# Performance work log

Measured on AMD Instinct MI355X. Metric: run time of the kernel, lower is better.

## Reference

```python
import jax, jax.numpy as jnp
import numpy as np
import math

D_MODEL = 1024
N_HEADS = 16
D_K = D_MODEL // N_HEADS
LN_EPS = 1e-5


def _linear_params(key, d_in, d_out):
    # torch Linear stores weight as [out, in]; xavier_uniform init
    bound = math.sqrt(6.0 / (d_in + d_out))
    kw, kb = jax.random.split(key)
    W = jax.random.uniform(kw, (d_out, d_in), jnp.float32, -bound, bound)
    b = jnp.zeros((d_out,), jnp.float32)
    return W, b


def setup_inputs() -> dict:
    key = jax.random.key(0)
    ks = jax.random.split(key, 8)
    x = jax.random.normal(ks[0], (2, 2048, D_MODEL), jnp.float32)
    reasoning_state = jax.random.normal(ks[1], (2, D_MODEL), jnp.float32)
    Wq, bq = _linear_params(ks[2], D_MODEL, D_MODEL)
    Wk, bk = _linear_params(ks[3], D_MODEL, D_MODEL)
    Wv, bv = _linear_params(ks[4], D_MODEL, D_MODEL)
    Wr, br = _linear_params(ks[5], D_MODEL, D_MODEL)
    Wo, bo = _linear_params(ks[6], D_MODEL, D_MODEL)
    ln_g = jnp.ones((D_MODEL,), jnp.float32)
    ln_b = jnp.zeros((D_MODEL,), jnp.float32)
    return {"x": x, "reasoning_state": reasoning_state,
            "Wq": Wq, "bq": bq, "Wk": Wk, "bk": bk, "Wv": Wv, "bv": bv,
            "Wr": Wr, "br": br, "Wo": Wo, "bo": bo, "ln_g": ln_g, "ln_b": ln_b}


def reference(x, reasoning_state, Wq, bq, Wk, bk, Wv, bv, Wr, br, Wo, bo, ln_g, ln_b):
    B, S, D = x.shape
    H, dk = N_HEADS, D_K

    def proj(z, W, b):  # torch Linear: z @ W.T + b
        return z @ W.T + b

    # [B, H, S, dk]
    Q = proj(x, Wq, bq).reshape(B, S, H, dk).transpose(0, 2, 1, 3)
    K = proj(x, Wk, bk).reshape(B, S, H, dk).transpose(0, 2, 1, 3)
    V = proj(x, Wv, bv).reshape(B, S, H, dk).transpose(0, 2, 1, 3)

    scores = jnp.einsum('bhsd,bhtd->bhst', Q, K) / math.sqrt(dk)

    # reasoning bias: R is [B, H, 1, dk]; Q @ R^T -> [B, H, S, 1], broadcast over keys
    R = proj(reasoning_state, Wr, br).reshape(B, 1, H, dk).transpose(0, 2, 1, 3)
    scores = scores + jnp.einsum('bhsd,bhud->bhsu', Q, R)  # u == 1, broadcasts

    attn = jax.nn.softmax(scores, axis=-1)
    context = jnp.einsum('bhst,bhtd->bshd', attn, V).reshape(B, S, D)
    out = proj(context, Wo, bo)

    # residual + LayerNorm
    y = out + x
    mu = jnp.mean(y, axis=-1, keepdims=True)
    var = jnp.var(y, axis=-1, keepdims=True)
    y = (y - mu) * jax.lax.rsqrt(var + LN_EPS) * ln_g + ln_b
    return (y, attn)
```

## Files before the change

### kernel.cpp

```cpp
#include <hip/hip_runtime.h>
#include <hip/hip_bf16.h>

#define DM 1024
#define NH 16
#define DKK 64
#define SL 2048
#define NBATCH 2
#define NR (NBATCH*SL)

typedef __attribute__((ext_vector_type(8))) __bf16 bf16x8;
typedef __attribute__((ext_vector_type(4))) float f32x4;
using bf16 = __hip_bfloat16;

#define QSCALE 0.18033688011112042f

#define LGKM_BARRIER() do { \
  asm volatile("s_waitcnt lgkmcnt(0)" ::: "memory"); \
  __builtin_amdgcn_s_barrier(); \
  __builtin_amdgcn_sched_barrier(0); \
} while (0)

__global__ __launch_bounds__(256) void cvt_kernel(const float* __restrict__ src,
                                                  bf16* __restrict__ dst, int n4) {
  int stride = gridDim.x * blockDim.x;
  for (int i = blockIdx.x * blockDim.x + threadIdx.x; i < n4; i += stride) {
    float4 v = ((const float4*)src)[i];
    union { bf16 h[4]; ushort4 u; } un;
    un.h[0] = __float2bfloat16(v.x);
    un.h[1] = __float2bfloat16(v.y);
    un.h[2] = __float2bfloat16(v.z);
    un.h[3] = __float2bfloat16(v.w);
    ((ushort4*)dst)[i] = un.u;
  }
}

__global__ __launch_bounds__(256) void cvt4_kernel(
    const float* __restrict__ s0, const float* __restrict__ s1,
    const float* __restrict__ s2, const float* __restrict__ s3,
    bf16* __restrict__ d0, bf16* __restrict__ d1,
    bf16* __restrict__ d2, bf16* __restrict__ d3) {
  const int z = blockIdx.y;
  const float* src = (z == 0) ? s0 : (z == 1) ? s1 : (z == 2) ? s2 : s3;
  bf16* dst = (z == 0) ? d0 : (z == 1) ? d1 : (z == 2) ? d2 : d3;
  const int n4 = DM * DM / 4;
  int stride = gridDim.x * blockDim.x;
  for (int i = blockIdx.x * blockDim.x + threadIdx.x; i < n4; i += stride) {
    float4 v = ((const float4*)src)[i];
    union { bf16 h[4]; ushort4 u; } un;
    un.h[0] = __float2bfloat16(v.x);
    un.h[1] = __float2bfloat16(v.y);
    un.h[2] = __float2bfloat16(v.z);
    un.h[3] = __float2bfloat16(v.w);
    ((ushort4*)dst)[i] = un.u;
  }
}

__device__ __forceinline__ void gemm_core(const bf16* __restrict__ A, const bf16* __restrict__ W,
                                          int rowStart, int colStart,
                                          bf16* As, bf16* Bs, f32x4 acc[4][4]) {
  const int t = threadIdx.x;
  const int lane = t & 63, w = t >> 6;
  const int lg = lane & 15, lh = lane >> 4;
  const int wm = (w >> 1) * 64, wn = (w & 1) * 64;
#pragma unroll
  for (int i = 0; i < 4; ++i)
#pragma unroll
    for (int j = 0; j < 4; ++j) acc[i][j] = (f32x4){0.f, 0.f, 0.f, 0.f};

  for (int kt = 0; kt < DM / 32; ++kt) {
    int kb = kt * 32;
#pragma unroll
    for (int q = 0; q < 2; ++q) {
      int idx = q * 256 + t;
      int row = idx >> 2;
      int ce = (idx & 3) * 8;
      const bf16* ga = A + (size_t)(rowStart + row) * DM + kb + ce;
      const bf16* gb = W + (size_t)(colStart + row) * DM + kb + ce;
      int ldsbase = (q * 256 + w * 64) * 8;
      __builtin_amdgcn_global_load_lds((const __attribute__((address_space(1))) void*)ga,
                                       (__attribute__((address_space(3))) void*)(As + ldsbase),
                                       16, 0, 0);
      __builtin_amdgcn_global_load_lds((const __attribute__((address_space(1))) void*)gb,
                                       (__attribute__((address_space(3))) void*)(Bs + ldsbase),
                                       16, 0, 0);
    }
    __syncthreads();
    bf16x8 af[4], bfr[4];
#pragma unroll
    for (int i = 0; i < 4; ++i)
      af[i] = *(const bf16x8*)(As + (wm + i * 16 + lg) * 32 + 8 * lh);
#pragma unroll
    for (int j = 0; j < 4; ++j)
      bfr[j] = *(const bf16x8*)(Bs + (wn + j * 16 + lg) * 32 + 8 * lh);
#pragma unroll
    for (int i = 0; i < 4; ++i)
#pragma unroll
      for (int j = 0; j < 4; ++j)
        acc[i][j] = __builtin_amdgcn_mfma_f32_16x16x32_bf16(af[i], bfr[j], acc[i][j], 0, 0, 0);
    __syncthreads();
  }
}

__global__ __launch_bounds__(256) void gemm_qkv_kernel(
    const bf16* __restrict__ xb,
    const bf16* __restrict__ Wqb, const bf16* __restrict__ Wkb, const bf16* __restrict__ Wvb,
    const float* __restrict__ bq, const float* __restrict__ bk, const float* __restrict__ bv,
    bf16* __restrict__ Qb, bf16* __restrict__ Kb, bf16* __restrict__ Vt) {
  __shared__ bf16 smem[128 * 128];
  bf16* As = smem;
  bf16* Bs = smem + 4096;
  const int z = blockIdx.z;
  const bf16* W = (z == 0) ? Wqb : (z == 1) ? Wkb : Wvb;
  const float* bias = (z == 0) ? bq : (z == 1) ? bk : bv;
  int rowStart = blockIdx.y * 128, colStart = blockIdx.x * 128;
  f32x4 acc[4][4];
  gemm_core(xb, W, rowStart, colStart, As, Bs, acc);

  const int t = threadIdx.x, lane = t & 63, w = t >> 6;
  const int lg = lane & 15, lh = lane >> 4;
  const int wm = (w >> 1) * 64, wn = (w & 1) * 64;
  if (z < 2) {
    bf16* out = (z == 0) ? Qb : Kb;
    const float sc = (z == 0) ? QSCALE : 1.0f;
#pragma unroll
    for (int i = 0; i < 4; ++i)
#pragma unroll
      for (int j = 0; j < 4; ++j) {
        int col = colStart + wn + j * 16 + lg;
        float bb = bias[col];
#pragma unroll
        for (int r = 0; r < 4; ++r) {
          int row = rowStart + wm + i * 16 + 4 * lh + r;
          out[(size_t)row * DM + col] = __float2bfloat16((acc[i][j][r] + bb) * sc);
        }
      }
  } else {
    char* T = (char*)smem;
    __syncthreads();
#pragma unroll
    for (int i = 0; i < 4; ++i)
#pragma unroll
      for (int j = 0; j < 4; ++j) {
        int col = wn + j * 16 + lg;
        float bb = bias[colStart + col];
        const int swz = (col & 7) << 4;
#pragma unroll
        for (int r2 = 0; r2 < 4; r2 += 2) {
          int row = wm + i * 16 + 4 * lh + r2;
          union { bf16 hh[2]; unsigned u; } un;
          un.hh[0] = __float2bfloat16(acc[i][j][r2] + bb);
          un.hh[1] = __float2bfloat16(acc[i][j][r2 + 1] + bb);
          *(unsigned*)(T + ((col * 256 + row * 2) ^ swz)) = un.u;
        }
      }
    __syncthreads();
    const int b_i = rowStart >> 11;
    const int sbase = rowStart & 2047;
#pragma unroll
    for (int rd = 0; rd < 8; ++rd) {
      int d_loc = rd * 16 + (t >> 4);
      int s8 = (t & 15) * 8;
      bf16x8 v = *(const bf16x8*)(T + ((d_loc * 256 + s8 * 2) ^ ((d_loc & 7) << 4)));
      int col = colStart + d_loc;
      int h2 = col >> 6, d = col & 63;
      *(bf16x8*)(Vt + ((size_t)(b_i * NH + h2) * DKK + d) * SL + sbase + s8) = v;
    }
  }
}

__global__ __launch_bounds__(256) void attn_den_kernel(
    const bf16* __restrict__ Qb, const bf16* __restrict__ Kb,
    float* __restrict__ linv_g) {
  __shared__ float sl[2 * 128];
  const int t = threadIdx.x, lane = t & 63, w = t >> 6;
  const int lg = lane & 15, lh = lane >> 4;
  const int L = blockIdx.x;
  const int xcd = L & 7, s_in = L >> 3;
  const int bh = xcd * 4 + (s_in >> 4);
  const int qtile = s_in & 15;
  const int b = bh >> 4, h = bh & 15;
  const int qbase = qtile * 128;
  const int wr = w >> 1, wc = w & 1;

  bf16x8 qf[4][2];
#pragma unroll
  for (int i = 0; i < 4; ++i)
#pragma unroll
    for (int ks = 0; ks < 2; ++ks)
      qf[i][ks] = *(const bf16x8*)(Qb +
          (size_t)(b * SL + qbase + wr * 64 + i * 16 + lg) * DM + h * DKK + ks * 32 + 8 * lh);

  const bf16* Kbase = Kb + (size_t)b * SL * DM + h * DKK;

  float lsum[4] = {0.f, 0.f, 0.f, 0.f};
  for (int kt = 0; kt < 16; ++kt) {
    bf16x8 kf[4][2];
#pragma unroll
    for (int j = 0; j < 4; ++j)
#pragma unroll
      for (int ks = 0; ks < 2; ++ks)
        kf[j][ks] = *(const bf16x8*)(Kbase +
            (size_t)(kt * 128 + wc * 64 + j * 16 + lg) * DM + ks * 32 + 8 * lh);
#pragma unroll
    for (int i = 0; i < 4; ++i) {
      f32x4 s[4];
      __builtin_amdgcn_s_setprio(1);
#pragma unroll
      for (int j = 0; j < 4; ++j) {
        f32x4 z = (f32x4){0.f, 0.f, 0.f, 0.f};
        z = __builtin_amdgcn_mfma_f32_16x16x32_bf16(kf[j][0], qf[i][0], z, 0, 0, 0);
        s[j] = __builtin_amdgcn_mfma_f32_16x16x32_bf16(kf[j][1], qf[i][1], z, 0, 0, 0);
      }
      __builtin_amdgcn_s_setprio(0);
#pragma unroll
      for (int j = 0; j < 4; ++j)
#pragma unroll
        for (int r = 0; r < 4; ++r) lsum[i] += exp2f(s[j][r]);
      __builtin_amdgcn_sched_barrier(0);
    }
  }
#pragma unroll
  for (int i = 0; i < 4; ++i) {
    lsum[i] += __shfl_xor(lsum[i], 16);
    lsum[i] += __shfl_xor(lsum[i], 32);
  }
  if (lh == 0) {
#pragma unroll
    for (int i = 0; i < 4; ++i) sl[wc * 128 + wr * 64 + i * 16 + lg] = lsum[i];
  }
  __syncthreads();
  if (t < 128) {
    linv_g[(size_t)bh * SL + qbase + t] = 1.f / (sl[t] + sl[128 + t]);
  }
}

__global__ __launch_bounds__(256) void attn_wr_kernel(
    const bf16* __restrict__ Qb, const bf16* __restrict__ Kb, const bf16* __restrict__ Vt,
    const float* __restrict__ linv_g,
    float* __restrict__ attn_out, bf16* __restrict__ ctxb) {
  __shared__ bf16 Ps[128 * 128];
  const int t = threadIdx.x, lane = t & 63, w = t >> 6;
  const int lg = lane & 15, lh = lane >> 4;
  const int L = blockIdx.x;
  const int xcd = L & 7, s_in = L >> 3;
  const int bh = xcd * 4 + (s_in >> 4);
  const int qtile = s_in & 15;
  const int b = bh >> 4, h = bh & 15;
  const int qbase = qtile * 128;
  const int wr = w >> 1, wc = w & 1;

  bf16x8 qf[4][2];
#pragma unroll
  for (int i = 0; i < 4; ++i)
#pragma unroll
    for (int ks = 0; ks < 2; ++ks)
      qf[i][ks] = *(const bf16x8*)(Qb +
          (size_t)(b * SL + qbase + wr * 64 + i * 16 + lg) * DM + h * DKK + ks * 32 + 8 * lh);

  float linv[4];
#pragma unroll
  for (int i = 0; i < 4; ++i)
    linv[i] = linv_g[(size_t)bh * SL + qbase + wr * 64 + i * 16 + lg];

  const bf16* Kbase = Kb + (size_t)b * SL * DM + h * DKK;
  const bf16* Vtb = Vt + (size_t)bh * DKK * SL;
  float* attn_base = attn_out + (size_t)bh * SL * SL;
  char* Pb = (char*)Ps;

  f32x4 cacc[4][2];
#pragma unroll
  for (int i = 0; i < 4; ++i) {
    cacc[i][0] = (f32x4){0.f, 0.f, 0.f, 0.f};
    cacc[i][1] = (f32x4){0.f, 0.f, 0.f, 0.f};
  }

  for (int kt = 0; kt < 16; ++kt) {
    bf16x8 kf[4][2];
#pragma unroll
    for (int j = 0; j < 4; ++j)
#pragma unroll
      for (int ks = 0; ks < 2; ++ks)
        kf[j][ks] = *(const bf16x8*)(Kbase +
            (size_t)(kt * 128 + wc * 64 + j * 16 + lg) * DM + ks * 32 + 8 * lh);

    LGKM_BARRIER();

#pragma unroll
    for (int i = 0; i < 4; ++i) {
      f32x4 s[4];
      __builtin_amdgcn_s_setprio(1);
#pragma unroll
      for (int j = 0; j < 4; ++j) {
        f32x4 z = (f32x4){0.f, 0.f, 0.f, 0.f};
        z = __builtin_amdgcn_mfma_f32_16x16x32_bf16(kf[j][0], qf[i][0], z, 0, 0, 0);
        s[j] = __builtin_amdgcn_mfma_f32_16x16x32_bf16(kf[j][1], qf[i][1], z, 0, 0, 0);
      }
      __builtin_amdgcn_s_setprio(0);
      const int q = wr * 64 + i * 16 + lg;
      const int swz = (q & 7) << 4;
#pragma unroll
      for (int j = 0; j < 4; ++j) {
        const int sk0 = wc * 64 + j * 16 + 4 * lh;
        f32x4 p4;
        p4[0] = exp2f(s[j][0]) * linv[i];
        p4[1] = exp2f(s[j][1]) * linv[i];
        p4[2] = exp2f(s[j][2]) * linv[i];
        p4[3] = exp2f(s[j][3]) * linv[i];
        __builtin_nontemporal_store(p4,
            (f32x4*)(attn_base + (size_t)(qbase + q) * SL + kt * 128 + sk0));
        union { bf16 hh[4]; ushort4 u4; } un;
        un.hh[0] = __float2bfloat16(p4[0]);
        un.hh[1] = __float2bfloat16(p4[1]);
        un.hh[2] = __float2bfloat16(p4[2]);
        un.hh[3] = __float2bfloat16(p4[3]);
        *(ushort4*)(Pb + ((q * 256 + sk0 * 2) ^ swz)) = un.u4;
      }
      __builtin_amdgcn_sched_barrier(0);
    }

    LGKM_BARRIER();

    __builtin_amdgcn_s_setprio(1);
#pragma unroll
    for (int ks = 0; ks < 4; ++ks) {
      bf16x8 pf[4];
#pragma unroll
      for (int i = 0; i < 4; ++i) {
        const int q = wr * 64 + i * 16 + lg;
        pf[i] = *(const bf16x8*)(Pb + ((q * 256 + ks * 64 + lh * 16) ^ ((q & 7) << 4)));
      }
      bf16x8 vf[2];
#pragma unroll
      for (int jd = 0; jd < 2; ++jd)
        vf[jd] = *(const bf16x8*)(Vtb +
            (size_t)(wc * 32 + jd * 16 + lg) * SL + kt * 128 + ks * 32 + 8 * lh);
#pragma unroll
      for (int i = 0; i < 4; ++i)
#pragma unroll
        for (int jd = 0; jd < 2; ++jd)
          cacc[i][jd] = __builtin_amdgcn_mfma_f32_16x16x32_bf16(pf[i], vf[jd], cacc[i][jd], 0, 0, 0);
    }
    __builtin_amdgcn_s_setprio(0);
  }

#pragma unroll
  for (int i = 0; i < 4; ++i)
#pragma unroll
    for (int jd = 0; jd < 2; ++jd)
#pragma unroll
      for (int r = 0; r < 4; ++r) {
        int row = qbase + wr * 64 + i * 16 + 4 * lh + r;
        int d = wc * 32 + jd * 16 + lg;
        ctxb[(size_t)(b * SL + row) * DM + h * DKK + d] = __float2bfloat16(cacc[i][jd][r]);
      }
}

__global__ __launch_bounds__(256) void gemm_o_kernel(
    const bf16* __restrict__ ctxb, const bf16* __restrict__ Wob, const float* __restrict__ bo,
    const float* __restrict__ xf, float* __restrict__ ypre) {
  __shared__ bf16 As[128 * 32], Bs[64 * 32];
  const int t = threadIdx.x, lane = t & 63, w = t >> 6;
  const int lg = lane & 15, lh = lane >> 4;
  const int wm = (w >> 1) * 64, wn = (w & 1) * 32;
  int rowStart = blockIdx.y * 128, colStart = blockIdx.x * 64;
  f32x4 acc[4][2];
#pragma unroll
  for (int i = 0; i < 4; ++i)
#pragma unroll
    for (int j = 0; j < 2; ++j) acc[i][j] = (f32x4){0.f, 0.f, 0.f, 0.f};

  for (int kt = 0; kt < DM / 32; ++kt) {
    int kb = kt * 32;
#pragma unroll
    for (int q = 0; q < 2; ++q) {
      int idx = q * 256 + t;
      int row = idx >> 2;
      int ce = (idx & 3) * 8;
      const bf16* ga = ctxb + (size_t)(rowStart + row) * DM + kb + ce;
      int ldsbase = (q * 256 + w * 64) * 8;
      __builtin_amdgcn_global_load_lds((const __attribute__((address_space(1))) void*)ga,
                                       (__attribute__((address_space(3))) void*)(As + ldsbase),
                                       16, 0, 0);
    }
    {
      int row = t >> 2, ce = (t & 3) * 8;
      const bf16* gb = Wob + (size_t)(colStart + row) * DM + kb + ce;
      int ldsbase = (w * 64) * 8;
      __builtin_amdgcn_global_load_lds((const __attribute__((address_space(1))) void*)gb,
                                       (__attribute__((address_space(3))) void*)(Bs + ldsbase),
                                       16, 0, 0);
    }
    __syncthreads();
    bf16x8 af[4], bfr[2];
#pragma unroll
    for (int i = 0; i < 4; ++i)
      af[i] = *(const bf16x8*)(As + (wm + i * 16 + lg) * 32 + 8 * lh);
#pragma unroll
    for (int j = 0; j < 2; ++j)
      bfr[j] = *(const bf16x8*)(Bs + (wn + j * 16 + lg) * 32 + 8 * lh);
#pragma unroll
    for (int i = 0; i < 4; ++i)
#pragma unroll
      for (int j = 0; j < 2; ++j)
        acc[i][j] = __builtin_amdgcn_mfma_f32_16x16x32_bf16(af[i], bfr[j], acc[i][j], 0, 0, 0);
    __syncthreads();
  }
#pragma unroll
  for (int i = 0; i < 4; ++i)
#pragma unroll
    for (int j = 0; j < 2; ++j) {
      int col = colStart + wn + j * 16 + lg;
      float bb = bo[col];
#pragma unroll
      for (int r = 0; r < 4; ++r) {
        int row = rowStart + wm + i * 16 + 4 * lh + r;
        ypre[(size_t)row * DM + col] = acc[i][j][r] + bb + xf[(size_t)row * DM + col];
      }
    }
}

__global__ __launch_bounds__(256) void ln_kernel(const float* __restrict__ ypre,
                                                 const float* __restrict__ g,
                                                 const float* __restrict__ bta,
                                                 float* __restrict__ out) {
  int row = blockIdx.x;
  const float* yr = ypre + (size_t)row * DM;
  int t = threadIdx.x;
  float4 v = *(const float4*)(yr + t * 4);
  float s = v.x + v.y + v.z + v.w;
  float ss = v.x * v.x + v.y * v.y + v.z * v.z + v.w * v.w;
#pragma unroll
  for (int off = 1; off < 64; off <<= 1) {
    s += __shfl_xor(s, off);
    ss += __shfl_xor(ss, off);
  }
  __shared__ float red[8];
  int w = t >> 6, lane = t & 63;
  if (lane == 0) { red[w] = s; red[4 + w] = ss; }
  __syncthreads();
  s = red[0] + red[1] + red[2] + red[3];
  ss = red[4] + red[5] + red[6] + red[7];
  float mu = s * (1.f / (float)DM);
  float var = ss * (1.f / (float)DM) - mu * mu;
  float rstd = rsqrtf(var + 1e-5f);
  float4 gv = *(const float4*)(g + t * 4);
  float4 bv = *(const float4*)(bta + t * 4);
  float4 o;
  o.x = (v.x - mu) * rstd * gv.x + bv.x;
  o.y = (v.y - mu) * rstd * gv.y + bv.y;
  o.z = (v.z - mu) * rstd * gv.z + bv.z;
  o.w = (v.w - mu) * rstd * gv.w + bv.w;
  *(float4*)(out + (size_t)row * DM + t * 4) = o;
}

extern "C" void kernel_launch(void* const* d_in, const int* in_sizes, int n_in,
                              void* d_out, int out_size, void* d_ws, size_t ws_size,
                              hipStream_t stream) {
  (void)in_sizes; (void)n_in; (void)out_size; (void)ws_size;
  const float* x = (const float*)d_in[0];
  const float* Wq = (const float*)d_in[2];
  const float* bq = (const float*)d_in[3];
  const float* Wk = (const float*)d_in[4];
  const float* bk = (const float*)d_in[5];
  const float* Wv = (const float*)d_in[6];
  const float* bv = (const float*)d_in[7];
  const float* Wo = (const float*)d_in[10];
  const float* bo = (const float*)d_in[11];
  const float* ln_g = (const float*)d_in[12];
  const float* ln_b = (const float*)d_in[13];
  float* out = (float*)d_out;

  char* ws = (char*)d_ws;
  const size_t MB = 1ull << 20;
  bf16* xb   = (bf16*)(ws + 0 * MB);
  bf16* Wqb  = (bf16*)(ws + 8 * MB);
  bf16* Wkb  = (bf16*)(ws + 10 * MB);
  bf16* Wvb  = (bf16*)(ws + 12 * MB);
  bf16* Wob  = (bf16*)(ws + 14 * MB);
  bf16* Qb   = (bf16*)(ws + 16 * MB);
  bf16* Kb   = (bf16*)(ws + 24 * MB);
  bf16* Vt   = (bf16*)(ws + 32 * MB);
  bf16* ctxb = (bf16*)(ws + 40 * MB);
  float* ypre = (float*)(ws + 48 * MB);
  float* linv_g = (float*)(ws + 64 * MB);

  float* y_out = out;
  float* attn_out = out + (size_t)NR * DM;

  cvt_kernel<<<2048, 256, 0, stream>>>(x, xb, NR * DM / 4);
  cvt4_kernel<<<dim3(256, 4), 256, 0, stream>>>(Wq, Wk, Wv, Wo, Wqb, Wkb, Wvb, Wob);

  gemm_qkv_kernel<<<dim3(8, 32, 3), 256, 0, stream>>>(xb, Wqb, Wkb, Wvb, bq, bk, bv, Qb, Kb, Vt);
  attn_den_kernel<<<512, 256, 0, stream>>>(Qb, Kb, linv_g);
  attn_wr_kernel<<<512, 256, 0, stream>>>(Qb, Kb, Vt, linv_g, attn_out, ctxb);
  gemm_o_kernel<<<dim3(16, 32), 256, 0, stream>>>(ctxb, Wob, bo, x, ypre);
  ln_kernel<<<4096, 256, 0, stream>>>(ypre, ln_g, ln_b, y_out);
}
```

Measured before the change: 332.8 us.

## Give each wave private P tiles to drop block barriers in attention write kernel

The attention write kernel is repartitioned so each wave owns 32 query rows and all 128 keys per tile, rather than a 2x2 wave grid that shares a P tile in LDS. Each wave writes and reads only its own double-buffered LDS P slice, so the two block-wide lgkm barriers per key tile are removed. The scheduling priority hints and sched barriers in the row-sum kernel are also dropped. In exchange, every wave now loads all 128 K rows and all 64 V columns, which doubles the global/L2 traffic for K and V per wave. It also raises register pressure from kf[8][2] and s[8].

```diff
diff --git a/kernel.cpp b/kernel.cpp
--- a/kernel.cpp
+++ b/kernel.cpp
@@ -13,12 +13,6 @@
 using bf16 = __hip_bfloat16;
 
 #define QSCALE 0.18033688011112042f
-
-#define LGKM_BARRIER() do { \
-  asm volatile("s_waitcnt lgkmcnt(0)" ::: "memory"); \
-  __builtin_amdgcn_s_barrier(); \
-  __builtin_amdgcn_sched_barrier(0); \
-} while (0)
 
 __global__ __launch_bounds__(256) void cvt_kernel(const float* __restrict__ src,
                                                   bf16* __restrict__ dst, int n4) {
@@ -204,19 +198,16 @@
 #pragma unroll
     for (int i = 0; i < 4; ++i) {
       f32x4 s[4];
-      __builtin_amdgcn_s_setprio(1);
 #pragma unroll
       for (int j = 0; j < 4; ++j) {
         f32x4 z = (f32x4){0.f, 0.f, 0.f, 0.f};
         z = __builtin_amdgcn_mfma_f32_16x16x32_bf16(kf[j][0], qf[i][0], z, 0, 0, 0);
         s[j] = __builtin_amdgcn_mfma_f32_16x16x32_bf16(kf[j][1], qf[i][1], z, 0, 0, 0);
       }
-      __builtin_amdgcn_s_setprio(0);
 #pragma unroll
       for (int j = 0; j < 4; ++j)
 #pragma unroll
         for (int r = 0; r < 4; ++r) lsum[i] += exp2f(s[j][r]);
-      __builtin_amdgcn_sched_barrier(0);
     }
   }
 #pragma unroll
@@ -238,7 +229,7 @@
     const bf16* __restrict__ Qb, const bf16* __restrict__ Kb, const bf16* __restrict__ Vt,
     const float* __restrict__ linv_g,
     float* __restrict__ attn_out, bf16* __restrict__ ctxb) {
-  __shared__ bf16 Ps[128 * 128];
+  __shared__ bf16 Ps[4][2][32 * 128];
   const int t = threadIdx.x, lane = t & 63, w = t >> 6;
   const int lg = lane & 15, lh = lane >> 4;
   const int L = blockIdx.x;
@@ -246,111 +237,104 @@
   const int bh = xcd * 4 + (s_in >> 4);
   const int qtile = s_in & 15;
   const int b = bh >> 4, h = bh & 15;
-  const int qbase = qtile * 128;
-  const int wr = w >> 1, wc = w & 1;
-
-  bf16x8 qf[4][2];
-#pragma unroll
-  for (int i = 0; i < 4; ++i)
+  const int qb2 = qtile * 128 + w * 32;
+
+  bf16x8 qf[2][2];
+#pragma unroll
+  for (int i = 0; i < 2; ++i)
 #pragma unroll
     for (int ks = 0; ks < 2; ++ks)
       qf[i][ks] = *(const bf16x8*)(Qb +
-          (size_t)(b * SL + qbase + wr * 64 + i * 16 + lg) * DM + h * DKK + ks * 32 + 8 * lh);
-
-  float linv[4];
-#pragma unroll
-  for (int i = 0; i < 4; ++i)
-    linv[i] = linv_g[(size_t)bh * SL + qbase + wr * 64 + i * 16 + lg];
+          (size_t)(b * SL + qb2 + i * 16 + lg) * DM + h * DKK + ks * 32 + 8 * lh);
+
+  float linv[2];
+#pragma unroll
+  for (int i = 0; i < 2; ++i)
+    linv[i] = linv_g[(size_t)bh * SL + qb2 + i * 16 + lg];
 
   const bf16* Kbase = Kb + (size_t)b * SL * DM + h * DKK;
   const bf16* Vtb = Vt + (size_t)bh * DKK * SL;
   float* attn_base = attn_out + (size_t)bh * SL * SL;
-  char* Pb = (char*)Ps;
-
-  f32x4 cacc[4][2];
-#pragma unroll
-  for (int i = 0; i < 4; ++i) {
-    cacc[i][0] = (f32x4){0.f, 0.f, 0.f, 0.f};
-    cacc[i][1] = (f32x4){0.f, 0.f, 0.f, 0.f};
-  }
+
+  f32x4 cacc[2][4];
+#pragma unroll
+  for (int i = 0; i < 2; ++i)
+#pragma unroll
+    for (int jd = 0; jd < 4; ++jd) cacc[i][jd] = (f32x4){0.f, 0.f, 0.f, 0.f};
 
   for (int kt = 0; kt < 16; ++kt) {
-    bf16x8 kf[4][2];
-#pragma unroll
-    for (int j = 0; j < 4; ++j)
+    char* Pb = (char*)(&Ps[w][kt & 1][0]);
+    bf16x8 kf[8][2];
+#pragma unroll
+    for (int j = 0; j < 8; ++j)
 #pragma unroll
       for (int ks = 0; ks < 2; ++ks)
         kf[j][ks] = *(const bf16x8*)(Kbase +
-            (size_t)(kt * 128 + wc * 64 + j * 16 + lg) * DM + ks * 32 + 8 * lh);
-
-    LGKM_BARRIER();
-
-#pragma unroll
-    for (int i = 0; i < 4; ++i) {
-      f32x4 s[4];
+            (size_t)(kt * 128 + j * 16 + lg) * DM + ks * 32 + 8 * lh);
+
+#pragma unroll
+    for (int i = 0; i < 2; ++i) {
+      f32x4 s[8];
       __builtin_amdgcn_s_setprio(1);
 #pragma unroll
-      for (int j = 0; j < 4; ++j) {
+      for (int j = 0; j < 8; ++j) {
         f32x4 z = (f32x4){0.f, 0.f, 0.f, 0.f};
         z = __builtin_amdgcn_mfma_f32_16x16x32_bf16(kf[j][0], qf[i][0], z, 0, 0, 0);
         s[j] = __builtin_amdgcn_mfma_f32_16x16x32_bf16(kf[j][1], qf[i][1], z, 0, 0, 0);
       }
       __builtin_amdgcn_s_setprio(0);
-      const int q = wr * 64 + i * 16 + lg;
-      const int swz = (q & 7) << 4;
-#pragma unroll
-      for (int j = 0; j < 4; ++j) {
-        const int sk0 = wc * 64 + j * 16 + 4 * lh;
+      const int qloc = i * 16 + lg;
+      const int swz = (qloc & 7) << 4;
+#pragma unroll
+      for (int j = 0; j < 8; ++j) {
+        const int key0 = j * 16 + 4 * lh;
         f32x4 p4;
         p4[0] = exp2f(s[j][0]) * linv[i];
         p4[1] = exp2f(s[j][1]) * linv[i];
         p4[2] = exp2f(s[j][2]) * linv[i];
         p4[3] = exp2f(s[j][3]) * linv[i];
         __builtin_nontemporal_store(p4,
-            (f32x4*)(attn_base + (size_t)(qbase + q) * SL + kt * 128 + sk0));
+            (f32x4*)(attn_base + (size_t)(qb2 + qloc) * SL + kt * 128 + key0));
         union { bf16 hh[4]; ushort4 u4; } un;
         un.hh[0] = __float2bfloat16(p4[0]);
         un.hh[1] = __float2bfloat16(p4[1]);
         un.hh[2] = __float2bfloat16(p4[2]);
         un.hh[3] = __float2bfloat16(p4[3]);
-        *(ushort4*)(Pb + ((q * 256 + sk0 * 2) ^ swz)) = un.u4;
-      }
-      __builtin_amdgcn_sched_barrier(0);
-    }
-
-    LGKM_BARRIER();
+        *(ushort4*)(Pb + ((qloc * 256 + key0 * 2) ^ swz)) = un.u4;
+      }
+    }
 
     __builtin_amdgcn_s_setprio(1);
 #pragma unroll
     for (int ks = 0; ks < 4; ++ks) {
-      bf16x8 pf[4];
-#pragma unroll
-      for (int i = 0; i < 4; ++i) {
-        const int q = wr * 64 + i * 16 + lg;
-        pf[i] = *(const bf16x8*)(Pb + ((q * 256 + ks * 64 + lh * 16) ^ ((q & 7) << 4)));
-      }
-      bf16x8 vf[2];
-#pragma unroll
-      for (int jd = 0; jd < 2; ++jd)
+      bf16x8 pf[2];
+#pragma unroll
+      for (int i = 0; i < 2; ++i) {
+        const int qloc = i * 16 + lg;
+        pf[i] = *(const bf16x8*)(Pb + ((qloc * 256 + (ks * 32 + 8 * lh) * 2) ^ ((qloc & 7) << 4)));
+      }
+      bf16x8 vf[4];
+#pragma unroll
+      for (int jd = 0; jd < 4; ++jd)
         vf[jd] = *(const bf16x8*)(Vtb +
-            (size_t)(wc * 32 + jd * 16 + lg) * SL + kt * 128 + ks * 32 + 8 * lh);
-#pragma unroll
-      for (int i = 0; i < 4; ++i)
-#pragma unroll
-        for (int jd = 0; jd < 2; ++jd)
+            (size_t)(jd * 16 + lg) * SL + kt * 128 + ks * 32 + 8 * lh);
+#pragma unroll
+      for (int i = 0; i < 2; ++i)
+#pragma unroll
+        for (int jd = 0; jd < 4; ++jd)
           cacc[i][jd] = __builtin_amdgcn_mfma_f32_16x16x32_bf16(pf[i], vf[jd], cacc[i][jd], 0, 0, 0);
     }
     __builtin_amdgcn_s_setprio(0);
   }
 
 #pragma unroll
-  for (int i = 0; i < 4; ++i)
-#pragma unroll
-    for (int jd = 0; jd < 2; ++jd)
+  for (int i = 0; i < 2; ++i)
+#pragma unroll
+    for (int jd = 0; jd < 4; ++jd)
 #pragma unroll
       for (int r = 0; r < 4; ++r) {
-        int row = qbase + wr * 64 + i * 16 + 4 * lh + r;
-        int d = wc * 32 + jd * 16 + lg;
+        int row = qb2 + i * 16 + 4 * lh + r;
+        int d = jd * 16 + lg;
         ctxb[(size_t)(b * SL + row) * DM + h * DKK + d] = __float2bfloat16(cacc[i][jd][r]);
       }
 }
```

Measured after the change: 309.1 us. -7.1%, faster.
